# Optimization experiments

Measured on AMD Instinct MI355X. Metric: run time of the kernel, lower is better.

Reference implementation:

```python
import jax, jax.numpy as jnp
import numpy as np

NUM_HEADS = 8
HIDDEN = 8

def conv1x1(x, w):
    # x: [B,C,H,W], w: [O,C] -> [B,O,H,W]
    return jnp.einsum('oc,bchw->bohw', w, x)

def grid_sample_border(img, gx, gy):
    # Bilinear grid_sample, padding_mode='border', align_corners=True.
    # img: [B,C,H,W]; gx, gy: [B,H,W] normalized coords in [-1,1].
    B, C, H, W = img.shape
    ix = (gx + 1.0) * 0.5 * (W - 1)
    iy = (gy + 1.0) * 0.5 * (H - 1)
    x0f = jnp.floor(ix); y0f = jnp.floor(iy)
    wx = (ix - x0f)[..., None]; wy = (iy - y0f)[..., None]
    x0 = x0f.astype(jnp.int32); y0 = y0f.astype(jnp.int32)
    x0c = jnp.clip(x0, 0, W - 1); x1c = jnp.clip(x0 + 1, 0, W - 1)
    y0c = jnp.clip(y0, 0, H - 1); y1c = jnp.clip(y0 + 1, 0, H - 1)
    imt = jnp.transpose(img, (0, 2, 3, 1))  # [B,H,W,C]
    b = jnp.arange(B)[:, None, None]
    v00 = imt[b, y0c, x0c]; v01 = imt[b, y0c, x1c]
    v10 = imt[b, y1c, x0c]; v11 = imt[b, y1c, x1c]
    out = (v00 * (1 - wx) * (1 - wy) + v01 * wx * (1 - wy)
           + v10 * (1 - wx) * wy + v11 * wx * wy)
    return jnp.transpose(out, (0, 3, 1, 2))

def process_sub(cur, ref, Wq, Wk, Wv, Wver, Whor):
    B, C, H, W = cur.shape
    c = HIDDEN // NUM_HEADS  # per-head channel dim (=1)
    q = conv1x1(cur, Wq).reshape(B, NUM_HEADS, c, H, W)
    k = conv1x1(ref, Wk).reshape(B, NUM_HEADS, c, H, W)
    v = conv1x1(ref, Wv).reshape(B, NUM_HEADS, c, H, W)
    # vertical axial attention (each column w independent, attend over rows)
    a_ver = jax.nn.softmax(jnp.einsum('bkchw,bkclw->bkwhl', q, k), axis=-1)
    o_ver = jnp.einsum('bkwhl,bkclw->bkchw', a_ver, v).reshape(B, HIDDEN, H, W)
    o_ver = conv1x1(o_ver, Wver)[:, 0]  # [B,H,W]
    # horizontal axial attention (each row h independent, attend over cols)
    a_hor = jax.nn.softmax(jnp.einsum('bkchw,bkchl->bkhwl', q, k), axis=-1)
    o_hor = jnp.einsum('bkhwl,bkchl->bkchw', a_hor, v).reshape(B, HIDDEN, H, W)
    o_hor = conv1x1(o_hor, Whor)[:, 0]  # [B,H,W]
    # identity grid + flow
    ys = -1.0 + 2.0 * jnp.arange(H, dtype=cur.dtype) / max(float(H - 1), 1.0)
    xs = -1.0 + 2.0 * jnp.arange(W, dtype=cur.dtype) / max(float(W - 1), 1.0)
    gx = xs[None, None, :] + o_hor / ((W - 1.0) / 2.0)
    gy = ys[None, :, None] + o_ver / ((H - 1.0) / 2.0)
    return grid_sample_border(ref, gx, gy)

def _forward(cur_fea, ref_fea, Wq, Wk, Wv, Wver, Whor):
    B, C, H, W = cur_fea.shape
    def split(x):
        return jnp.stack([x[:, :, ::2, ::2], x[:, :, 1::2, 1::2],
                          x[:, :, ::2, 1::2], x[:, :, 1::2, ::2]], 0)
    cur_sub = split(cur_fea).reshape(4 * B, C, H // 2, W // 2)
    ref_sub = split(ref_fea).reshape(4 * B, C, H // 2, W // 2)
    warped = process_sub(cur_sub, ref_sub, Wq, Wk, Wv, Wver, Whor)
    ul, br, ur, bl = warped.reshape(4, B, C, H // 2, W // 2)
    out = jnp.zeros((B, C, H, W), dtype=jnp.float32)
    out = out.at[:, :, ::2, ::2].set(ul)
    out = out.at[:, :, ::2, 1::2].set(ur)
    out = out.at[:, :, 1::2, ::2].set(bl)
    out = out.at[:, :, 1::2, 1::2].set(br)
    return out

def setup_inputs() -> dict:
    key = jax.random.key(0)
    ks = jax.random.split(key, 7)
    B, C, H, W = 2, 64, 256, 256
    return {
        'cur_fea': jax.random.normal(ks[0], (B, C, H, W), jnp.float32),
        'ref_fea': jax.random.normal(ks[1], (B, C, H, W), jnp.float32),
        'Wq': jax.random.normal(ks[2], (HIDDEN, C), jnp.float32) * 0.05,
        'Wk': jax.random.normal(ks[3], (HIDDEN, C), jnp.float32) * 0.05,
        'Wv': jax.random.normal(ks[4], (HIDDEN, C), jnp.float32) * 0.05,
        'Wver': jax.random.normal(ks[5], (1, HIDDEN), jnp.float32) * 0.05,
        'Whor': jax.random.normal(ks[6], (1, HIDDEN), jnp.float32) * 0.05,
    }

def reference(cur_fea, ref_fea, Wq, Wk, Wv, Wver, Whor):
    return _forward(cur_fea, ref_fea, Wq, Wk, Wv, Wver, Whor)
```

## Files before the change

kernel.cpp:

```cpp
#include <hip/hip_runtime.h>


constexpr int PLANE = 16384;
constexpr float LOG2E = 1.4426950408889634f;

__global__ __launch_bounds__(256) void qkv_kernel(
    const float* __restrict__ cur, const float* __restrict__ ref,
    const float* __restrict__ Wq, const float* __restrict__ Wk,
    const float* __restrict__ Wv,
    float* __restrict__ Q, float* __restrict__ K, float* __restrict__ V)
{
    __shared__ float WT[64 * 24];
    __shared__ float red[128 * 25];
    const int tid = threadIdx.x;
    for (int i = tid; i < 64 * 24; i += 256) {
        int c = i / 24, j = i % 24;
        float val = (j < 8) ? Wq[j * 64 + c]
                  : (j < 16) ? Wk[(j - 8) * 64 + c]
                  : Wv[(j - 16) * 64 + c];
        WT[c * 24 + j] = val;
    }
    __syncthreads();

    const int bi = blockIdx.x;
    const int b  = bi >> 9;
    const int Y  = (bi >> 1) & 255;
    const int Xh = bi & 1;
    const int cg = tid >> 7;
    const int xi = tid & 127;
    const int X  = Xh * 128 + xi;

    const size_t base_in = (size_t)b * 64 * 65536 + (size_t)Y * 256 + X;
    const float* curp = cur + base_in;
    const float* refp = ref + base_in;

    float q[8], k[8], v[8];
#pragma unroll
    for (int i = 0; i < 8; ++i) { q[i] = 0.f; k[i] = 0.f; v[i] = 0.f; }

    const int c0 = cg * 32;
#pragma unroll 4
    for (int c = 0; c < 32; ++c) {
        float cu = curp[(size_t)(c0 + c) * 65536];
        float rf = refp[(size_t)(c0 + c) * 65536];
        const float* wr = &WT[(c0 + c) * 24];
#pragma unroll
        for (int i = 0; i < 8; ++i) {
            q[i] = fmaf(wr[i],      cu, q[i]);
            k[i] = fmaf(wr[8 + i],  rf, k[i]);
            v[i] = fmaf(wr[16 + i], rf, v[i]);
        }
    }

    if (cg) {
#pragma unroll
        for (int i = 0; i < 8; ++i) {
            red[xi * 25 + i]      = q[i];
            red[xi * 25 + 8 + i]  = k[i];
            red[xi * 25 + 16 + i] = v[i];
        }
    }
    __syncthreads();
    if (!cg) {
        const int dy = Y & 1, dx = X & 1;
        const int p  = dy ? (dx ? 1 : 3) : (dx ? 2 : 0);
        const int sb = p * 2 + b;
        const int h = Y >> 1, w = X >> 1;
#pragma unroll
        for (int i = 0; i < 8; ++i) {
            const size_t o = ((size_t)(sb * 8 + i) << 14) + (h << 7) + w;
            Q[o] = q[i] + red[xi * 25 + i];
            K[o] = k[i] + red[xi * 25 + 8 + i];
            V[o] = v[i] + red[xi * 25 + 16 + i];
        }
    }
}

__global__ __launch_bounds__(256) void transpose_kernel(
    const float* __restrict__ Q, const float* __restrict__ K,
    const float* __restrict__ V,
    float* __restrict__ QT, float* __restrict__ KT, float* __restrict__ VT)
{
    __shared__ float tile[32 * 33];
    const int bi = blockIdx.x;
    const int plane = bi >> 4;
    const int ti = (bi >> 2) & 3, tj = bi & 3;
    const int t = threadIdx.x;
    const int r = t >> 3, c4 = (t & 7) * 4;
    const size_t pb = (size_t)plane << 14;
    const size_t ibase = pb + (size_t)(ti * 32) * 128 + tj * 32;
    const size_t obase = pb + (size_t)(tj * 32) * 128 + ti * 32;

    const float* srcs[3] = { Q, K, V };
    float* dsts[3] = { QT, KT, VT };
#pragma unroll
    for (int a = 0; a < 3; ++a) {
        const float* src = srcs[a];
        float* dst = dsts[a];
        const float4 val = *(const float4*)&src[ibase + (size_t)r * 128 + c4];
        if (a) __syncthreads();
        tile[r * 33 + c4 + 0] = val.x;
        tile[r * 33 + c4 + 1] = val.y;
        tile[r * 33 + c4 + 2] = val.z;
        tile[r * 33 + c4 + 3] = val.w;
        __syncthreads();
        float4 o;
        o.x = tile[(c4 + 0) * 33 + r];
        o.y = tile[(c4 + 1) * 33 + r];
        o.z = tile[(c4 + 2) * 33 + r];
        o.w = tile[(c4 + 3) * 33 + r];
        *(float4*)&dst[obase + (size_t)r * 128 + c4] = o;
    }
}

__global__ __launch_bounds__(1024) void attn_axial(
    const float* __restrict__ Qa, const float* __restrict__ Ka,
    const float* __restrict__ Va, const float* __restrict__ wsel,
    float* __restrict__ o)
{
    __shared__ float kk[8 * 128];
    __shared__ float vv[8 * 128];
    __shared__ float red[8 * 128];

    const int tid  = threadIdx.x;
    const int head = tid >> 7;
    const int t    = tid & 127;
    const int sb   = blockIdx.x >> 7;
    const int line = blockIdx.x & 127;

    const size_t ph = ((size_t)(sb * 8 + head)) << 14;
    const size_t row = ph + ((size_t)line << 7);
    kk[tid] = LOG2E * Ka[row + t];
    vv[tid] = Va[row + t];
    const float s = Qa[row + t];
    __syncthreads();

    const float4* k4 = (const float4*)&kk[head << 7];
    const float4* v4 = (const float4*)&vv[head << 7];
    float d0 = 0.f, d1 = 0.f, d2 = 0.f, d3 = 0.f;
    float n0 = 0.f, n1 = 0.f, n2 = 0.f, n3 = 0.f;
#pragma unroll 8
    for (int l = 0; l < 32; ++l) {
        const float4 kq = k4[l];
        const float4 vq = v4[l];
        const float e0 = __builtin_amdgcn_exp2f(s * kq.x);
        const float e1 = __builtin_amdgcn_exp2f(s * kq.y);
        const float e2 = __builtin_amdgcn_exp2f(s * kq.z);
        const float e3 = __builtin_amdgcn_exp2f(s * kq.w);
        d0 += e0; n0 = fmaf(e0, vq.x, n0);
        d1 += e1; n1 = fmaf(e1, vq.y, n1);
        d2 += e2; n2 = fmaf(e2, vq.z, n2);
        d3 += e3; n3 = fmaf(e3, vq.w, n3);
    }
    const float den = (d0 + d1) + (d2 + d3);
    const float num = (n0 + n1) + (n2 + n3);
    red[tid] = num * __builtin_amdgcn_rcpf(den);
    __syncthreads();

    if (tid < 128) {
        float acc = 0.f;
#pragma unroll
        for (int i = 0; i < 8; ++i)
            acc = fmaf(wsel[i], red[(i << 7) + tid], acc);
        o[((size_t)sb << 14) + ((size_t)line << 7) + tid] = acc;
    }
}

__global__ __launch_bounds__(256) void warp_kernel(
    const float* __restrict__ ref, const float* __restrict__ ovt,
    const float* __restrict__ oh, float* __restrict__ out)
{
    const int g = blockIdx.x * 256 + threadIdx.x;
    const int chalf = g >> 17;
    const int pid = g & (131072 - 1);
    const int sb  = pid >> 14;
    const int pix = pid & (PLANE - 1);
    const int h = pix >> 7, w = pix & 127;
    const int p = sb >> 1, b = sb & 1;
    const int dy = p & 1, dx = (p == 1) | (p == 2);

    const float ix = (float)w + oh[pid];
    const float iy = (float)h + ovt[((size_t)sb << 14) + (w << 7) + h];

    const float x0f = floorf(ix), y0f = floorf(iy);
    const float wx = ix - x0f,    wy = iy - y0f;
    const int x0 = (int)x0f, y0 = (int)y0f;
    const int x0c = min(max(x0, 0), 127),     x1c = min(max(x0 + 1, 0), 127);
    const int y0c = min(max(y0, 0), 127),     y1c = min(max(y0 + 1, 0), 127);

    const float w00 = (1.f - wx) * (1.f - wy);
    const float w01 = wx * (1.f - wy);
    const float w10 = (1.f - wx) * wy;
    const float w11 = wx * wy;

    const int r0 = (2 * y0c + dy) * 256, r1 = (2 * y1c + dy) * 256;
    const int c0 = 2 * x0c + dx,         c1 = 2 * x1c + dx;
    const int o00 = r0 + c0, o01 = r0 + c1, o10 = r1 + c0, o11 = r1 + c1;
    const int dst = (2 * h + dy) * 256 + (2 * w + dx);

    const float* rp = ref + (size_t)b * 64 * 65536;
    float* op = out + (size_t)b * 64 * 65536;

    const int cbeg = chalf * 32;
#pragma unroll 4
    for (int c = 0; c < 32; ++c) {
        const size_t pl = (size_t)(cbeg + c) * 65536;
        const float v00 = rp[pl + o00], v01 = rp[pl + o01];
        const float v10 = rp[pl + o10], v11 = rp[pl + o11];
        op[pl + dst] = fmaf(w00, v00, fmaf(w01, v01, fmaf(w10, v10, w11 * v11)));
    }
}

extern "C" void kernel_launch(void* const* d_in, const int* in_sizes, int n_in,
                              void* d_out, int out_size, void* d_ws, size_t ws_size,
                              hipStream_t stream)
{
    const float* cur  = (const float*)d_in[0];
    const float* ref  = (const float*)d_in[1];
    const float* Wq   = (const float*)d_in[2];
    const float* Wk   = (const float*)d_in[3];
    const float* Wv   = (const float*)d_in[4];
    const float* Wver = (const float*)d_in[5];
    const float* Whor = (const float*)d_in[6];
    float* out = (float*)d_out;

    float* ws = (float*)d_ws;
    const size_t NQ = 8 * 8 * (size_t)PLANE;
    float* Q   = ws;
    float* K   = Q  + NQ;
    float* V   = K  + NQ;
    float* QT  = V  + NQ;
    float* KT  = QT + NQ;
    float* VT  = KT + NQ;
    float* OVT = VT + NQ;
    float* OH  = OVT + 8 * (size_t)PLANE;

    qkv_kernel<<<1024, 256, 0, stream>>>(cur, ref, Wq, Wk, Wv, Q, K, V);
    transpose_kernel<<<1024, 256, 0, stream>>>(Q, K, V, QT, KT, VT);
    attn_axial<<<1024, 1024, 0, stream>>>(Q,  K,  V,  Whor, OH);
    attn_axial<<<1024, 1024, 0, stream>>>(QT, KT, VT, Wver, OVT);
    warp_kernel<<<1024, 256, 0, stream>>>(ref, OVT, OH, out);
}
```

Baseline: 189.5 us.

## Split QKV channel reduction four ways, merge attention passes, remap warp threads

The QKV projection now uses 512 threads per block with four channel groups, combined by a two-stage shared-memory reduction. The two axial attention launches are merged into one 2048-block launch that picks its pass from the block index. The warp kernel is remapped so each block covers one full output row of 256 pixels for 16 channels, which makes stores contiguous. Together these aim to raise parallelism, cut launch overhead, and coalesce warp-kernel writes, at the cost of an extra barrier and more shared memory in the QKV kernel.

```diff
diff --git a/kernel.cpp b/kernel.cpp
--- a/kernel.cpp
+++ b/kernel.cpp
@@ -4,16 +4,17 @@
 constexpr int PLANE = 16384;
 constexpr float LOG2E = 1.4426950408889634f;
 
-__global__ __launch_bounds__(256) void qkv_kernel(
+__global__ __launch_bounds__(512) void qkv_kernel(
     const float* __restrict__ cur, const float* __restrict__ ref,
     const float* __restrict__ Wq, const float* __restrict__ Wk,
     const float* __restrict__ Wv,
     float* __restrict__ Q, float* __restrict__ K, float* __restrict__ V)
 {
     __shared__ float WT[64 * 24];
-    __shared__ float red[128 * 25];
+    __shared__ float red0[128 * 25];
+    __shared__ float red1[128 * 25];
     const int tid = threadIdx.x;
-    for (int i = tid; i < 64 * 24; i += 256) {
+    for (int i = tid; i < 64 * 24; i += 512) {
         int c = i / 24, j = i % 24;
         float val = (j < 8) ? Wq[j * 64 + c]
                   : (j < 16) ? Wk[(j - 8) * 64 + c]
@@ -38,9 +39,9 @@
 #pragma unroll
     for (int i = 0; i < 8; ++i) { q[i] = 0.f; k[i] = 0.f; v[i] = 0.f; }
 
-    const int c0 = cg * 32;
-#pragma unroll 4
-    for (int c = 0; c < 32; ++c) {
+    const int c0 = cg * 16;
+#pragma unroll 8
+    for (int c = 0; c < 16; ++c) {
         float cu = curp[(size_t)(c0 + c) * 65536];
         float rf = refp[(size_t)(c0 + c) * 65536];
         const float* wr = &WT[(c0 + c) * 24];
@@ -52,16 +53,35 @@
         }
     }
 
-    if (cg) {
-#pragma unroll
-        for (int i = 0; i < 8; ++i) {
-            red[xi * 25 + i]      = q[i];
-            red[xi * 25 + 8 + i]  = k[i];
-            red[xi * 25 + 16 + i] = v[i];
-        }
-    }
-    __syncthreads();
-    if (!cg) {
+    float* row0 = &red0[xi * 25];
+    float* row1 = &red1[xi * 25];
+    if (cg == 1) {
+#pragma unroll
+        for (int i = 0; i < 8; ++i) {
+            row0[i] = q[i]; row0[8 + i] = k[i]; row0[16 + i] = v[i];
+        }
+    } else if (cg == 3) {
+#pragma unroll
+        for (int i = 0; i < 8; ++i) {
+            row1[i] = q[i]; row1[8 + i] = k[i]; row1[16 + i] = v[i];
+        }
+    }
+    __syncthreads();
+    if (cg == 2) {
+#pragma unroll
+        for (int i = 0; i < 8; ++i) {
+            row1[i]      += q[i];
+            row1[8 + i]  += k[i];
+            row1[16 + i] += v[i];
+        }
+    } else if (cg == 0) {
+#pragma unroll
+        for (int i = 0; i < 8; ++i) {
+            q[i] += row0[i]; k[i] += row0[8 + i]; v[i] += row0[16 + i];
+        }
+    }
+    __syncthreads();
+    if (cg == 0) {
         const int dy = Y & 1, dx = X & 1;
         const int p  = dy ? (dx ? 1 : 3) : (dx ? 2 : 0);
         const int sb = p * 2 + b;
@@ -69,9 +89,9 @@
 #pragma unroll
         for (int i = 0; i < 8; ++i) {
             const size_t o = ((size_t)(sb * 8 + i) << 14) + (h << 7) + w;
-            Q[o] = q[i] + red[xi * 25 + i];
-            K[o] = k[i] + red[xi * 25 + 8 + i];
-            V[o] = v[i] + red[xi * 25 + 16 + i];
+            Q[o] = q[i] + row1[i];
+            K[o] = k[i] + row1[8 + i];
+            V[o] = v[i] + row1[16 + i];
         }
     }
 }
@@ -113,23 +133,33 @@
     }
 }
 
-__global__ __launch_bounds__(1024) void attn_axial(
-    const float* __restrict__ Qa, const float* __restrict__ Ka,
-    const float* __restrict__ Va, const float* __restrict__ wsel,
-    float* __restrict__ o)
+__global__ __launch_bounds__(1024) void attn_fused(
+    const float* __restrict__ Q, const float* __restrict__ K,
+    const float* __restrict__ V,
+    const float* __restrict__ QT, const float* __restrict__ KT,
+    const float* __restrict__ VT,
+    const float* __restrict__ Whor, const float* __restrict__ Wver,
+    float* __restrict__ OH, float* __restrict__ OVT)
 {
     __shared__ float kk[8 * 128];
     __shared__ float vv[8 * 128];
     __shared__ float red[8 * 128];
 
+    const int pass = blockIdx.x >> 10;
+    const float* __restrict__ Qa = pass ? QT : Q;
+    const float* __restrict__ Ka = pass ? KT : K;
+    const float* __restrict__ Va = pass ? VT : V;
+    const float* __restrict__ wsel = pass ? Wver : Whor;
+    float* __restrict__ o = pass ? OVT : OH;
+
     const int tid  = threadIdx.x;
     const int head = tid >> 7;
     const int t    = tid & 127;
-    const int sb   = blockIdx.x >> 7;
-    const int line = blockIdx.x & 127;
-
-    const size_t ph = ((size_t)(sb * 8 + head)) << 14;
-    const size_t row = ph + ((size_t)line << 7);
+    const int sbl  = blockIdx.x & 1023;
+    const int sb   = sbl >> 7;
+    const int line = sbl & 127;
+
+    const size_t row = (((size_t)(sb * 8 + head)) << 14) + ((size_t)line << 7);
     kk[tid] = LOG2E * Ka[row + t];
     vv[tid] = Va[row + t];
     const float s = Qa[row + t];
@@ -170,16 +200,18 @@
     const float* __restrict__ ref, const float* __restrict__ ovt,
     const float* __restrict__ oh, float* __restrict__ out)
 {
-    const int g = blockIdx.x * 256 + threadIdx.x;
-    const int chalf = g >> 17;
-    const int pid = g & (131072 - 1);
-    const int sb  = pid >> 14;
-    const int pix = pid & (PLANE - 1);
-    const int h = pix >> 7, w = pix & 127;
-    const int p = sb >> 1, b = sb & 1;
-    const int dy = p & 1, dx = (p == 1) | (p == 2);
-
-    const float ix = (float)w + oh[pid];
+    const int bi = blockIdx.x;
+    const int Y  = bi & 255;
+    const int cg = (bi >> 8) & 3;
+    const int b  = bi >> 10;
+    const int X  = threadIdx.x;
+
+    const int dy = Y & 1, dx = X & 1;
+    const int p  = dy ? (dx ? 1 : 3) : (dx ? 2 : 0);
+    const int sb = p * 2 + b;
+    const int h = Y >> 1, w = X >> 1;
+
+    const float ix = (float)w + oh [((size_t)sb << 14) + (h << 7) + w];
     const float iy = (float)h + ovt[((size_t)sb << 14) + (w << 7) + h];
 
     const float x0f = floorf(ix), y0f = floorf(iy);
@@ -196,15 +228,14 @@
     const int r0 = (2 * y0c + dy) * 256, r1 = (2 * y1c + dy) * 256;
     const int c0 = 2 * x0c + dx,         c1 = 2 * x1c + dx;
     const int o00 = r0 + c0, o01 = r0 + c1, o10 = r1 + c0, o11 = r1 + c1;
-    const int dst = (2 * h + dy) * 256 + (2 * w + dx);
-
-    const float* rp = ref + (size_t)b * 64 * 65536;
-    float* op = out + (size_t)b * 64 * 65536;
-
-    const int cbeg = chalf * 32;
+    const int dst = Y * 256 + X;
+
+    const float* rp = ref + ((size_t)b * 64 + cg * 16) * 65536;
+    float* op = out + ((size_t)b * 64 + cg * 16) * 65536;
+
 #pragma unroll 4
-    for (int c = 0; c < 32; ++c) {
-        const size_t pl = (size_t)(cbeg + c) * 65536;
+    for (int c = 0; c < 16; ++c) {
+        const size_t pl = (size_t)c * 65536;
         const float v00 = rp[pl + o00], v01 = rp[pl + o01];
         const float v10 = rp[pl + o10], v11 = rp[pl + o11];
         op[pl + dst] = fmaf(w00, v00, fmaf(w01, v01, fmaf(w10, v10, w11 * v11)));
@@ -235,9 +266,9 @@
     float* OVT = VT + NQ;
     float* OH  = OVT + 8 * (size_t)PLANE;
 
-    qkv_kernel<<<1024, 256, 0, stream>>>(cur, ref, Wq, Wk, Wv, Q, K, V);
+    qkv_kernel<<<1024, 512, 0, stream>>>(cur, ref, Wq, Wk, Wv, Q, K, V);
     transpose_kernel<<<1024, 256, 0, stream>>>(Q, K, V, QT, KT, VT);
-    attn_axial<<<1024, 1024, 0, stream>>>(Q,  K,  V,  Whor, OH);
-    attn_axial<<<1024, 1024, 0, stream>>>(QT, KT, VT, Wver, OVT);
-    warp_kernel<<<1024, 256, 0, stream>>>(ref, OVT, OH, out);
-}
+    attn_fused<<<2048, 1024, 0, stream>>>(Q, K, V, QT, KT, VT,
+                                          Whor, Wver, OH, OVT);
+    warp_kernel<<<2048, 256, 0, stream>>>(ref, OVT, OH, out);
+}
```

Measured after the change: 199.9 us. 5.5% more time.
